# Performance work log

Measured on AMD Instinct MI355X. Metric: run time of the kernel, lower is better.

## Reference

```python
import jax, jax.numpy as jnp
import numpy as np

SEQ, B, I, H = 2048, 64, 512, 512

def setup_inputs() -> dict:
    key = jax.random.key(0)
    k1, k2, k3 = jax.random.split(key, 3)
    return {
        "input": jax.random.normal(k1, (SEQ, B, I), dtype=jnp.float32),
        "hx": jnp.zeros((1, B, H), dtype=jnp.float32),
        "weight_ih": jax.random.normal(k2, (H, I), dtype=jnp.float32) * 0.01,
        "weight_hh": jax.random.normal(k3, (H, H), dtype=jnp.float32) * 0.01,
        "bias_ih": jnp.zeros((H,), dtype=jnp.float32),
        "bias_hh": jnp.zeros((H,), dtype=jnp.float32),
    }

def reference(input, hx, weight_ih, weight_hh, bias_ih, bias_hh):
    # Batch the input-side projection across all timesteps in one GEMM:
    # [S,B,I] @ [I,H] -> [S,B,H]
    x_proj = jnp.einsum('sbi,hi->sbh', input, weight_ih) + bias_ih + bias_hh
    h0 = hx[0]  # [B,H]

    def step(h, xp_t):
        h_new = jnp.tanh(xp_t + h @ weight_hh.T)
        return h_new, h_new

    h_last, outputs = jax.lax.scan(step, h0, x_proj)
    return outputs, h_last[None]
```

## Files before the change

### kernel.cpp

```cpp
#include <hip/hip_runtime.h>
#include <stdint.h>

#define S_LEN 2048
#define B_SZ  64
#define I_SZ  512
#define H_SZ  512

typedef __attribute__((ext_vector_type(8))) short bf16x8;
typedef __attribute__((ext_vector_type(4))) float f32x4;

__device__ __forceinline__ uint16_t f2b(float x) {
    uint32_t u = __float_as_uint(x);
    uint32_t r = (u + 0x7fffu + ((u >> 16) & 1u)) >> 16;
    return (uint16_t)r;
}

__global__ void cvt_weights_kernel(const float* __restrict__ wih,
                                   const float* __restrict__ whh,
                                   uint16_t* __restrict__ wihb,
                                   uint16_t* __restrict__ whhb) {
    int i = (blockIdx.x * blockDim.x + threadIdx.x) * 4;
    float4 a = *reinterpret_cast<const float4*>(wih + i);
    float4 b = *reinterpret_cast<const float4*>(whh + i);
    union { uint16_t u[4]; uint2 v; } pa, pb;
    pa.u[0] = f2b(a.x); pa.u[1] = f2b(a.y); pa.u[2] = f2b(a.z); pa.u[3] = f2b(a.w);
    pb.u[0] = f2b(b.x); pb.u[1] = f2b(b.y); pb.u[2] = f2b(b.z); pb.u[3] = f2b(b.w);
    *reinterpret_cast<uint2*>(wihb + i) = pa.v;
    *reinterpret_cast<uint2*>(whhb + i) = pb.v;
}

#define BM 128
#define BN 128
#define BK 32

__launch_bounds__(256)
__global__ void xproj_gemm_kernel(const float* __restrict__ inp,
                                  const uint16_t* __restrict__ wihb,
                                  const float* __restrict__ bih,
                                  const float* __restrict__ bhh,
                                  float* __restrict__ xp)
{
    __shared__ __align__(16) uint16_t Asm[2][BM * BK];
    __shared__ __align__(16) uint16_t Bsm[2][BN * BK];

    const int tid  = threadIdx.x;
    const int lane = tid & 63;
    const int w    = tid >> 6;
    const int wm   = (w >> 1) * 64;
    const int wn   = (w & 1) * 64;
    const int bid  = blockIdx.x;
    const int m0   = (bid >> 2) * BM;
    const int n0   = (bid & 3) * BN;

    const int srow  = tid >> 1;
    const int shalf = (tid & 1) * 16;

    float bsum[4];
#pragma unroll
    for (int nn = 0; nn < 4; ++nn) {
        int col = n0 + wn + nn * 16 + (lane & 15);
        bsum[nn] = bih[col] + bhh[col];
    }

    f32x4 acc[4][4];
#pragma unroll
    for (int mm = 0; mm < 4; ++mm)
#pragma unroll
        for (int nn = 0; nn < 4; ++nn)
            acc[mm][nn] = f32x4{0.f, 0.f, 0.f, 0.f};

    float4 ar[4];
    bf16x8 br[2];

    auto loadA = [&](int kt) {
        const float* g = inp + (size_t)(m0 + srow) * I_SZ + kt * BK + shalf;
#pragma unroll
        for (int q = 0; q < 4; ++q) ar[q] = *reinterpret_cast<const float4*>(g + q * 4);
    };
    auto loadB = [&](int kt) {
        const uint16_t* g = wihb + (size_t)(n0 + srow) * I_SZ + kt * BK + shalf;
        br[0] = *reinterpret_cast<const bf16x8*>(g);
        br[1] = *reinterpret_cast<const bf16x8*>(g + 8);
    };
    auto writeA = [&](int buf) {
        alignas(16) uint16_t tmp[16];
#pragma unroll
        for (int q = 0; q < 4; ++q) {
            tmp[q * 4 + 0] = f2b(ar[q].x); tmp[q * 4 + 1] = f2b(ar[q].y);
            tmp[q * 4 + 2] = f2b(ar[q].z); tmp[q * 4 + 3] = f2b(ar[q].w);
        }
        *reinterpret_cast<bf16x8*>(&Asm[buf][srow * BK + shalf])     = *reinterpret_cast<bf16x8*>(tmp);
        *reinterpret_cast<bf16x8*>(&Asm[buf][srow * BK + shalf + 8]) = *reinterpret_cast<bf16x8*>(tmp + 8);
    };
    auto writeB = [&](int buf) {
        *reinterpret_cast<bf16x8*>(&Bsm[buf][srow * BK + shalf])     = br[0];
        *reinterpret_cast<bf16x8*>(&Bsm[buf][srow * BK + shalf + 8]) = br[1];
    };

    loadA(0); loadB(0); writeA(0); writeB(0);
    __syncthreads();

    for (int kt = 0; kt < I_SZ / BK; ++kt) {
        const int cur = kt & 1;
        const bool more = (kt + 1) < I_SZ / BK;
        if (more) { loadA(kt + 1); loadB(kt + 1); }

        bf16x8 afrag[4], bfrag[4];
#pragma unroll
        for (int mm = 0; mm < 4; ++mm)
            afrag[mm] = *reinterpret_cast<const bf16x8*>(
                &Asm[cur][(wm + mm * 16 + (lane & 15)) * BK + (lane >> 4) * 8]);
#pragma unroll
        for (int nn = 0; nn < 4; ++nn)
            bfrag[nn] = *reinterpret_cast<const bf16x8*>(
                &Bsm[cur][(wn + nn * 16 + (lane & 15)) * BK + (lane >> 4) * 8]);
#pragma unroll
        for (int mm = 0; mm < 4; ++mm)
#pragma unroll
            for (int nn = 0; nn < 4; ++nn)
                acc[mm][nn] = __builtin_amdgcn_mfma_f32_16x16x32_bf16(
                    afrag[mm], bfrag[nn], acc[mm][nn], 0, 0, 0);

        if (more) { writeA(cur ^ 1); writeB(cur ^ 1); }
        __syncthreads();
    }

#pragma unroll
    for (int mm = 0; mm < 4; ++mm) {
        const int rbase = m0 + wm + mm * 16 + (lane >> 4) * 4;
#pragma unroll
        for (int nn = 0; nn < 4; ++nn) {
            const int col = n0 + wn + nn * 16 + (lane & 15);
#pragma unroll
            for (int r = 0; r < 4; ++r)
                xp[(size_t)(rbase + r) * H_SZ + col] = acc[mm][nn][r] + bsum[nn];
        }
    }
}

__launch_bounds__(512, 2)
__global__ void rnn_rec_kernel(const uint16_t* __restrict__ whhb,
                               const float* __restrict__ hx,
                               float* __restrict__ out)
{
    __shared__ __align__(16) uint16_t Asm[8 * 16 * 512];
    __shared__ __align__(16) uint16_t hsm[512];
    __shared__ __align__(16) float    ysm[512];

    const int tid  = threadIdx.x;
    const int lane = tid & 63;
    const int w    = tid >> 6;
    const int b    = blockIdx.x;
    const int r16  = lane & 15;
    const int q    = lane >> 4;

    bf16x8 areg[48];
#pragma unroll
    for (int jt = 0; jt < 3; ++jt)
#pragma unroll
        for (int kt = 0; kt < 16; ++kt)
            areg[jt * 16 + kt] = *reinterpret_cast<const bf16x8*>(
                whhb + (size_t)(w * 64 + jt * 16 + r16) * H_SZ + kt * 32 + q * 8);
#pragma unroll
    for (int kt = 0; kt < 16; ++kt)
        *reinterpret_cast<bf16x8*>(&Asm[(w * 16 + kt) * 512 + lane * 8]) =
            *reinterpret_cast<const bf16x8*>(
                whhb + (size_t)(w * 64 + 48 + r16) * H_SZ + kt * 32 + q * 8);

    hsm[tid] = f2b(hx[(size_t)b * H_SZ + tid]);
    float xp_next = out[(size_t)b * H_SZ + tid];
    __syncthreads();

    for (int s = 0; s < S_LEN; ++s) {
        f32x4 a0{0.f,0.f,0.f,0.f}, a1{0.f,0.f,0.f,0.f}, a2{0.f,0.f,0.f,0.f}, a3{0.f,0.f,0.f,0.f};
#pragma unroll
        for (int kt = 0; kt < 16; ++kt) {
            bf16x8 bf = *reinterpret_cast<const bf16x8*>(&hsm[kt * 32 + q * 8]);
            bf16x8 al = *reinterpret_cast<const bf16x8*>(&Asm[(w * 16 + kt) * 512 + lane * 8]);
            a0 = __builtin_amdgcn_mfma_f32_16x16x32_bf16(areg[kt],      bf, a0, 0, 0, 0);
            a1 = __builtin_amdgcn_mfma_f32_16x16x32_bf16(areg[16 + kt], bf, a1, 0, 0, 0);
            a2 = __builtin_amdgcn_mfma_f32_16x16x32_bf16(areg[32 + kt], bf, a2, 0, 0, 0);
            a3 = __builtin_amdgcn_mfma_f32_16x16x32_bf16(al,            bf, a3, 0, 0, 0);
        }
        if (r16 == 0) {
#pragma unroll
            for (int r = 0; r < 4; ++r) {
                ysm[w * 64 +  0 + q * 4 + r] = a0[r];
                ysm[w * 64 + 16 + q * 4 + r] = a1[r];
                ysm[w * 64 + 32 + q * 4 + r] = a2[r];
                ysm[w * 64 + 48 + q * 4 + r] = a3[r];
            }
        }
        __syncthreads();

        float v  = ysm[tid] + xp_next;
        float e  = __expf(2.f * v);
        float th = 1.f - 2.f / (e + 1.f);
        out[((size_t)s * B_SZ + b) * H_SZ + tid] = th;
        if (s + 1 < S_LEN)
            xp_next = out[((size_t)(s + 1) * B_SZ + b) * H_SZ + tid];
        hsm[tid] = f2b(th);
        if (s == S_LEN - 1)
            out[(size_t)S_LEN * B_SZ * H_SZ + (size_t)b * H_SZ + tid] = th;
        __syncthreads();
    }
}

extern "C" void kernel_launch(void* const* d_in, const int* in_sizes, int n_in,
                              void* d_out, int out_size, void* d_ws, size_t ws_size,
                              hipStream_t stream) {
    const float* inp = (const float*)d_in[0];
    const float* hx  = (const float*)d_in[1];
    const float* wih = (const float*)d_in[2];
    const float* whh = (const float*)d_in[3];
    const float* bih = (const float*)d_in[4];
    const float* bhh = (const float*)d_in[5];
    float* out = (float*)d_out;

    uint16_t* wihb = (uint16_t*)d_ws;
    uint16_t* whhb = wihb + (size_t)H_SZ * I_SZ;

    cvt_weights_kernel<<<256, 256, 0, stream>>>(wih, whh, wihb, whhb);

    const int grid_gemm = (S_LEN * B_SZ / BM) * (H_SZ / BN);
    xproj_gemm_kernel<<<grid_gemm, 256, 0, stream>>>(inp, wihb, bih, bhh, out);

    rnn_rec_kernel<<<B_SZ, 512, 0, stream>>>(whhb, hx, out);
}
```

Before: 3.348 ms.

## Apply tanh in MFMA registers and double-buffer hidden state to halve barriers

In the recurrent kernel, each step now applies tanh straight from the MFMA accumulators. Lanes with r16<4 take one of the four tiles, write float4 outputs and pack bf16 hidden values into a double-buffered LDS hidden state. This removes the ysm staging round-trip and one of the two block barriers per timestep, and the loop is unrolled by two. The input projection is prefetched two steps ahead. The final h_last is read back from the bf16 buffer, so it carries bf16 rounding instead of the full float value.

After: 4.848 ms. 44.8% more time.

```diff
diff --git a/kernel.cpp b/kernel.cpp
--- a/kernel.cpp
+++ b/kernel.cpp
@@ -13,6 +13,11 @@
     uint32_t u = __float_as_uint(x);
     uint32_t r = (u + 0x7fffu + ((u >> 16) & 1u)) >> 16;
     return (uint16_t)r;
+}
+
+__device__ __forceinline__ float tfun(float v) {
+    float e = __expf(2.f * v);
+    return 1.f - 2.f / (e + 1.f);
 }
 
 __global__ void cvt_weights_kernel(const float* __restrict__ wih,
@@ -138,14 +143,43 @@
     }
 }
 
-__launch_bounds__(512, 2)
+
+#define STEP(P, XP, sidx)                                                                   \
+  {                                                                                          \
+    f32x4 c0{0.f,0.f,0.f,0.f}, c1{0.f,0.f,0.f,0.f}, c2{0.f,0.f,0.f,0.f}, c3{0.f,0.f,0.f,0.f};\
+    _Pragma("unroll")                                                                        \
+    for (int kt = 0; kt < 16; ++kt) {                                                        \
+      bf16x8 bf = *reinterpret_cast<const bf16x8*>(&hsm[P][kt * 32 + q * 8]);                \
+      bf16x8 al = *reinterpret_cast<const bf16x8*>(&Asm[(w * 16 + kt) * 512 + lane * 8]);    \
+      c0 = __builtin_amdgcn_mfma_f32_16x16x32_bf16(areg[kt],      bf, c0, 0, 0, 0);          \
+      c1 = __builtin_amdgcn_mfma_f32_16x16x32_bf16(areg[16 + kt], bf, c1, 0, 0, 0);          \
+      c2 = __builtin_amdgcn_mfma_f32_16x16x32_bf16(areg[32 + kt], bf, c2, 0, 0, 0);          \
+      c3 = __builtin_amdgcn_mfma_f32_16x16x32_bf16(al,            bf, c3, 0, 0, 0);          \
+    }                                                                                        \
+    if (act) {                                                                               \
+      f32x4 my = (c == 0) ? c0 : ((c == 1) ? c1 : ((c == 2) ? c2 : c3));                     \
+      float t0 = tfun(my[0] + XP.x), t1 = tfun(my[1] + XP.y);                                \
+      float t2 = tfun(my[2] + XP.z), t3 = tfun(my[3] + XP.w);                                \
+      *reinterpret_cast<float4*>(out + ((size_t)(sidx) * B_SZ + b) * H_SZ + j0) =            \
+          make_float4(t0, t1, t2, t3);                                                       \
+      uint2 hp;                                                                              \
+      hp.x = (uint32_t)f2b(t0) | ((uint32_t)f2b(t1) << 16);                                  \
+      hp.y = (uint32_t)f2b(t2) | ((uint32_t)f2b(t3) << 16);                                  \
+      *reinterpret_cast<uint2*>(&hsm[(P) ^ 1][j0]) = hp;                                     \
+      int prow = ((sidx) + 2 <= S_LEN) ? ((sidx) + 2) : 0;                                   \
+      XP = *reinterpret_cast<const float4*>(out + ((size_t)prow * B_SZ + b) * H_SZ + j0);    \
+    }                                                                                        \
+    asm volatile("s_waitcnt lgkmcnt(0)" ::: "memory");                                       \
+    __builtin_amdgcn_s_barrier();                                                            \
+  }
+
+__launch_bounds__(512, 1)
 __global__ void rnn_rec_kernel(const uint16_t* __restrict__ whhb,
                                const float* __restrict__ hx,
                                float* __restrict__ out)
 {
     __shared__ __align__(16) uint16_t Asm[8 * 16 * 512];
-    __shared__ __align__(16) uint16_t hsm[512];
-    __shared__ __align__(16) float    ysm[512];
+    __shared__ __align__(16) uint16_t hsm[2][512];
 
     const int tid  = threadIdx.x;
     const int lane = tid & 63;
@@ -167,43 +201,27 @@
             *reinterpret_cast<const bf16x8*>(
                 whhb + (size_t)(w * 64 + 48 + r16) * H_SZ + kt * 32 + q * 8);
 
-    hsm[tid] = f2b(hx[(size_t)b * H_SZ + tid]);
-    float xp_next = out[(size_t)b * H_SZ + tid];
+    hsm[0][tid] = f2b(hx[(size_t)b * H_SZ + tid]);
+
+    const int  c   = r16;
+    const bool act = (r16 < 4);
+    const int  j0  = w * 64 + c * 16 + q * 4;
+
+    float4 xpA = make_float4(0.f, 0.f, 0.f, 0.f);
+    float4 xpB = make_float4(0.f, 0.f, 0.f, 0.f);
+    if (act) {
+        xpA = *reinterpret_cast<const float4*>(out + ((size_t)0 * B_SZ + b) * H_SZ + j0);
+        xpB = *reinterpret_cast<const float4*>(out + ((size_t)1 * B_SZ + b) * H_SZ + j0);
+    }
     __syncthreads();
 
-    for (int s = 0; s < S_LEN; ++s) {
-        f32x4 a0{0.f,0.f,0.f,0.f}, a1{0.f,0.f,0.f,0.f}, a2{0.f,0.f,0.f,0.f}, a3{0.f,0.f,0.f,0.f};
-#pragma unroll
-        for (int kt = 0; kt < 16; ++kt) {
-            bf16x8 bf = *reinterpret_cast<const bf16x8*>(&hsm[kt * 32 + q * 8]);
-            bf16x8 al = *reinterpret_cast<const bf16x8*>(&Asm[(w * 16 + kt) * 512 + lane * 8]);
-            a0 = __builtin_amdgcn_mfma_f32_16x16x32_bf16(areg[kt],      bf, a0, 0, 0, 0);
-            a1 = __builtin_amdgcn_mfma_f32_16x16x32_bf16(areg[16 + kt], bf, a1, 0, 0, 0);
-            a2 = __builtin_amdgcn_mfma_f32_16x16x32_bf16(areg[32 + kt], bf, a2, 0, 0, 0);
-            a3 = __builtin_amdgcn_mfma_f32_16x16x32_bf16(al,            bf, a3, 0, 0, 0);
-        }
-        if (r16 == 0) {
-#pragma unroll
-            for (int r = 0; r < 4; ++r) {
-                ysm[w * 64 +  0 + q * 4 + r] = a0[r];
-                ysm[w * 64 + 16 + q * 4 + r] = a1[r];
-                ysm[w * 64 + 32 + q * 4 + r] = a2[r];
-                ysm[w * 64 + 48 + q * 4 + r] = a3[r];
-            }
-        }
-        __syncthreads();
-
-        float v  = ysm[tid] + xp_next;
-        float e  = __expf(2.f * v);
-        float th = 1.f - 2.f / (e + 1.f);
-        out[((size_t)s * B_SZ + b) * H_SZ + tid] = th;
-        if (s + 1 < S_LEN)
-            xp_next = out[((size_t)(s + 1) * B_SZ + b) * H_SZ + tid];
-        hsm[tid] = f2b(th);
-        if (s == S_LEN - 1)
-            out[(size_t)S_LEN * B_SZ * H_SZ + (size_t)b * H_SZ + tid] = th;
-        __syncthreads();
-    }
+    for (int s = 0; s < S_LEN; s += 2) {
+        STEP(0, xpA, s);
+        STEP(1, xpB, s + 1);
+    }
+
+    uint32_t u = hsm[0][tid];
+    out[(size_t)S_LEN * B_SZ * H_SZ + (size_t)b * H_SZ + tid] = __uint_as_float(u << 16);
 }
 
 extern "C" void kernel_launch(void* const* d_in, const int* in_sizes, int n_in,
```
